# Performance work log

Measured on AMD Instinct MI355X. Metric: run time of the kernel, lower is better.

## Reference

```python
import jax, jax.numpy as jnp
import numpy as np

NH, DH, DM = 16, 128, 2048
ROPE_THETA = 10000.0


def setup_inputs() -> dict:
    key = jax.random.key(0)
    k1, k2, k3 = jax.random.split(key, 3)
    x = jax.random.normal(k1, (2, 2048, DM), dtype=jnp.float32)
    w_qkv = jax.random.normal(k2, (3 * DM, DM), dtype=jnp.float32) * (DM ** -0.5)
    w_op = jax.random.normal(k3, (DM, DM), dtype=jnp.float32) * (DM ** -0.5)
    return {"x": x, "w_qkv": w_qkv, "w_op": w_op}


def _rope_tables(T, dtype):
    inv_freq = 1.0 / (ROPE_THETA ** (jnp.arange(0, DH, 2, dtype=jnp.float32) / DH))
    t = jnp.arange(T, dtype=jnp.float32)
    freqs = jnp.outer(t, inv_freq)              # (T, DH/2)
    emb = jnp.concatenate([freqs, freqs], axis=-1)  # (T, DH)
    cos = jnp.cos(emb)[None, :, None, :].astype(dtype)  # (1,T,1,DH)
    sin = jnp.sin(emb)[None, :, None, :].astype(dtype)
    return cos, sin


def _rotate_half(a):
    a1, a2 = a[..., : DH // 2], a[..., DH // 2 :]
    return jnp.concatenate([-a2, a1], axis=-1)


def reference(x, w_qkv, w_op):
    B, T, D = x.shape
    qkv = jnp.einsum('btd,ed->bte', x, w_qkv).reshape(B, T, 3, NH, DH)
    q, k, v = qkv[:, :, 0], qkv[:, :, 1], qkv[:, :, 2]  # (B,T,NH,DH)

    cos, sin = _rope_tables(T, x.dtype)
    q = q * cos + _rotate_half(q) * sin
    k = k * cos + _rotate_half(k) * sin

    # causal scaled dot-product attention
    scale = 1.0 / jnp.sqrt(jnp.asarray(DH, dtype=x.dtype))
    scores = jnp.einsum('bqhd,bkhd->bhqk', q, k) * scale  # (B,NH,T,T)
    causal = jnp.tril(jnp.ones((T, T), dtype=bool))
    scores = jnp.where(causal[None, None], scores, jnp.asarray(-1e30, dtype=x.dtype))
    attn = jax.nn.softmax(scores, axis=-1)
    out = jnp.einsum('bhqk,bkhd->bqhd', attn, v).reshape(B, T, D)
    return jnp.einsum('btd,ed->bte', out, w_op)
```

## Files before the change

### kernel.cpp

```cpp
#include <hip/hip_runtime.h>
#include <hip/hip_bf16.h>
#include <cstdint>

#define NHEAD 16
#define DHEAD 128
#define DMODEL 2048
#define TSEQ 2048
#define BATCH 2

using bf16 = __hip_bfloat16;
typedef __attribute__((ext_vector_type(4))) float  f32x4;
typedef __attribute__((ext_vector_type(2))) float  f32x2;
typedef __attribute__((ext_vector_type(4))) float  float4_t;
typedef __attribute__((ext_vector_type(4))) short  s16x4;
typedef __bf16 bf16x8 __attribute__((ext_vector_type(8)));

#define GLOAD_LDS16(gptr, lptr)                                                        \
  __builtin_amdgcn_global_load_lds((const __attribute__((address_space(1))) void*)(gptr), \
                                   (__attribute__((address_space(3))) void*)(lptr), 16, 0, 0)

#if __has_builtin(__builtin_amdgcn_exp2f)
#define EXP2(x) __builtin_amdgcn_exp2f(x)
#else
#define EXP2(x) exp2f(x)
#endif

__device__ __forceinline__ float bf2f(bf16 v) { return __bfloat162float(v); }
__device__ __forceinline__ bf16  f2bf(float f) { return __float2bfloat16(f); }
__device__ __forceinline__ unsigned short bfbits(float f) {
  return __builtin_bit_cast(unsigned short, f2bf(f));
}
__device__ __forceinline__ unsigned int pack2(float a, float b) {
  return (unsigned int)bfbits(a) | ((unsigned int)bfbits(b) << 16);
}

__global__ void cast_f32_to_bf16(const float* __restrict__ in, unsigned short* __restrict__ out, int n4) {
  int stride = gridDim.x * blockDim.x;
  for (int i = blockIdx.x * blockDim.x + threadIdx.x; i < n4; i += stride) {
    float4_t v = reinterpret_cast<const float4_t*>(in)[i];
    s16x4 r;
    r.x = (short)bfbits(v.x);
    r.y = (short)bfbits(v.y);
    r.z = (short)bfbits(v.z);
    r.w = (short)bfbits(v.w);
    reinterpret_cast<s16x4*>(out)[i] = r;
  }
}

__global__ void rope_tables(f32x2* __restrict__ cstab) {
  int i = blockIdx.x * blockDim.x + threadIdx.x;
  if (i >= TSEQ * 64) return;
  int t = i >> 6, f = i & 63;
  float inv = __expf(-((2.0f * (float)f) / 128.0f) * logf(10000.0f));
  float ang = (float)t * inv;
  f32x2 cs;
  cs.x = cosf(ang);
  cs.y = sinf(ang);
  cstab[i] = cs;
}

__global__ void transpose_v(const unsigned short* __restrict__ qkv, unsigned short* __restrict__ vt) {
  __shared__ short tile[64][132];
  const int bh = blockIdx.y;
  const int b = bh >> 4, h = bh & 15;
  const int t0 = blockIdx.x * 64;
  const int tid = threadIdx.x;
#pragma unroll
  for (int p = 0; p < 8; ++p) {
    int row  = p * 8 + (tid >> 5);
    int col  = (tid & 31) * 4;
    const unsigned short* src = qkv + (size_t)(b * TSEQ + t0 + row) * (3 * DMODEL) + 2 * DMODEL + h * DHEAD + col;
    s16x4 v = *reinterpret_cast<const s16x4*>(src);
    *reinterpret_cast<s16x4*>(&tile[row][col]) = v;
  }
  __syncthreads();
#pragma unroll
  for (int q = 0; q < 8; ++q) {
    int idx = q * 256 + tid;
    int d = idx >> 4, tq = idx & 15;
    s16x4 r;
    r.x = tile[tq * 4 + 0][d];
    r.y = tile[tq * 4 + 1][d];
    r.z = tile[tq * 4 + 2][d];
    r.w = tile[tq * 4 + 3][d];
    *reinterpret_cast<s16x4*>(vt + (size_t)(bh * DHEAD + d) * TSEQ + t0 + tq * 4) = r;
  }
}

__device__ __forceinline__ void store_c(float* p, float v) { *p = v; }
__device__ __forceinline__ void store_c(unsigned short* p, float v) { *p = bfbits(v); }

template <typename CT, bool ROPE>
__global__ __launch_bounds__(512, 2) void gemm_8p(const unsigned short* __restrict__ A,
                                                  const unsigned short* __restrict__ B,
                                                  CT* __restrict__ C, int M, int N, int K,
                                                  const f32x2* __restrict__ cstab) {
  __shared__ __align__(16) unsigned short As[2][256 * 64];
  __shared__ __align__(16) unsigned short Bs[2][256 * 64];

  const int tid  = threadIdx.x;
  const int lane = tid & 63;
  const int wave = tid >> 6;
  const int lrow = lane >> 4, lcol = lane & 15;
  const int wm2 = wave >> 2, wn4 = wave & 3;

  const int cpx = gridDim.x >> 3;
  const int bid = (blockIdx.x & 7) * cpx + (blockIdx.x >> 3);
  const int nby = N >> 8;
  const int m0 = (bid / nby) * 256;
  const int n0 = (bid % nby) * 256;
  const int NT = K >> 6;

  f32x4 acc[8][4] = {};

#define STAGE_M(MAT, DST, slot, k0)                                          \
  {                                                                          \
    _Pragma("unroll")                                                        \
    for (int it_ = 0; it_ < 4; ++it_) {                                      \
      int CC_ = it_ * 512 + tid;                                             \
      int R_ = CC_ >> 3, c_ = CC_ & 7;                                       \
      GLOAD_LDS16(MAT + (size_t)((DST) + R_) * K + (k0) + ((c_ ^ (R_ & 7)) << 3), \
                  (char*)(&slot[0]) + CC_ * 16);                             \
    }                                                                        \
  }

#define RD_FRAG(BASE, R, ks)                                                 \
  (*reinterpret_cast<const bf16x8*>(                                         \
      (BASE) + (R) * 128 + (((((ks) << 2) + lrow) ^ (lcol & 7)) << 4)))

  STAGE_M(A, m0, As[0], 0);
  STAGE_M(B, n0, Bs[0], 0);
  __syncthreads();

  for (int t = 0; t < NT; ++t) {
    const char* Ab = (const char*)(&As[t & 1][0]);
    const char* Bb = (const char*)(&Bs[t & 1][0]);
    const bool pf = (t + 1 < NT);
    const int psl = (t + 1) & 1;
    const int pk0 = (t + 1) << 6;

    bf16x8 af[4][2], bfr[2][2];

#pragma unroll
    for (int mf = 0; mf < 4; ++mf)
#pragma unroll
      for (int ks = 0; ks < 2; ++ks)
        af[mf][ks] = RD_FRAG(Ab, wm2 * 128 + mf * 16 + lcol, ks);
#pragma unroll
    for (int si = 0; si < 2; ++si)
#pragma unroll
      for (int ks = 0; ks < 2; ++ks)
        bfr[si][ks] = RD_FRAG(Bb, (wn4 + 4 * si) * 16 + lcol, ks);
    if (pf) STAGE_M(A, m0, As[psl], pk0);
    __builtin_amdgcn_s_barrier();
    __builtin_amdgcn_sched_barrier(0);
    __builtin_amdgcn_s_setprio(1);
#pragma unroll
    for (int mf = 0; mf < 4; ++mf)
#pragma unroll
      for (int si = 0; si < 2; ++si)
#pragma unroll
        for (int ks = 0; ks < 2; ++ks)
          acc[mf][si] = __builtin_amdgcn_mfma_f32_16x16x32_bf16(af[mf][ks], bfr[si][ks], acc[mf][si], 0, 0, 0);
    __builtin_amdgcn_s_setprio(0);
    __builtin_amdgcn_s_barrier();
    __builtin_amdgcn_sched_barrier(0);

#pragma unroll
    for (int si = 0; si < 2; ++si)
#pragma unroll
      for (int ks = 0; ks < 2; ++ks)
        bfr[si][ks] = RD_FRAG(Bb, (wn4 + 4 * (2 + si)) * 16 + lcol, ks);
    if (pf) STAGE_M(B, n0, Bs[psl], pk0);
    __builtin_amdgcn_s_barrier();
    __builtin_amdgcn_sched_barrier(0);
    __builtin_amdgcn_s_setprio(1);
#pragma unroll
    for (int mf = 0; mf < 4; ++mf)
#pragma unroll
      for (int si = 0; si < 2; ++si)
#pragma unroll
        for (int ks = 0; ks < 2; ++ks)
          acc[mf][2 + si] = __builtin_amdgcn_mfma_f32_16x16x32_bf16(af[mf][ks], bfr[si][ks], acc[mf][2 + si], 0, 0, 0);
    __builtin_amdgcn_s_setprio(0);
    __builtin_amdgcn_s_barrier();
    __builtin_amdgcn_sched_barrier(0);

#pragma unroll
    for (int mf = 0; mf < 4; ++mf)
#pragma unroll
      for (int ks = 0; ks < 2; ++ks)
        af[mf][ks] = RD_FRAG(Ab, wm2 * 128 + (4 + mf) * 16 + lcol, ks);
    __builtin_amdgcn_s_barrier();
    __builtin_amdgcn_sched_barrier(0);
    __builtin_amdgcn_s_setprio(1);
#pragma unroll
    for (int mf = 0; mf < 4; ++mf)
#pragma unroll
      for (int si = 0; si < 2; ++si)
#pragma unroll
        for (int ks = 0; ks < 2; ++ks)
          acc[4 + mf][2 + si] = __builtin_amdgcn_mfma_f32_16x16x32_bf16(af[mf][ks], bfr[si][ks], acc[4 + mf][2 + si], 0, 0, 0);
    __builtin_amdgcn_s_setprio(0);
    __builtin_amdgcn_s_barrier();
    __builtin_amdgcn_sched_barrier(0);

#pragma unroll
    for (int si = 0; si < 2; ++si)
#pragma unroll
      for (int ks = 0; ks < 2; ++ks)
        bfr[si][ks] = RD_FRAG(Bb, (wn4 + 4 * si) * 16 + lcol, ks);
    __builtin_amdgcn_s_barrier();
    __builtin_amdgcn_sched_barrier(0);
    __builtin_amdgcn_s_setprio(1);
#pragma unroll
    for (int mf = 0; mf < 4; ++mf)
#pragma unroll
      for (int si = 0; si < 2; ++si)
#pragma unroll
        for (int ks = 0; ks < 2; ++ks)
          acc[4 + mf][si] = __builtin_amdgcn_mfma_f32_16x16x32_bf16(af[mf][ks], bfr[si][ks], acc[4 + mf][si], 0, 0, 0);
    __builtin_amdgcn_s_setprio(0);

    __syncthreads();
  }
#undef STAGE_M
#undef RD_FRAG

  if (ROPE && n0 < 2 * DMODEL) {
    const float qsc = (n0 < DMODEL) ? 0.12751743f : 1.0f;
    const int f = wn4 * 16 + lcol;
#pragma unroll
    for (int mi = 0; mi < 8; ++mi)
#pragma unroll
      for (int j = 0; j < 4; ++j) {
        const int r = m0 + wm2 * 128 + mi * 16 + lrow * 4 + j;
        const int t = r & (TSEQ - 1);
        const f32x2 cs = cstab[t * 64 + f];
        const float a1 = acc[mi][0][j], a2 = acc[mi][1][j];
        store_c(C + (size_t)r * N + n0 + f,       (a1 * cs.x - a2 * cs.y) * qsc);
        store_c(C + (size_t)r * N + n0 + f + 64,  (a2 * cs.x + a1 * cs.y) * qsc);
        const float b1 = acc[mi][2][j], b2 = acc[mi][3][j];
        store_c(C + (size_t)r * N + n0 + f + 128, (b1 * cs.x - b2 * cs.y) * qsc);
        store_c(C + (size_t)r * N + n0 + f + 192, (b2 * cs.x + b1 * cs.y) * qsc);
      }
  } else {
#pragma unroll
    for (int mi = 0; mi < 8; ++mi)
#pragma unroll
      for (int si = 0; si < 4; ++si)
#pragma unroll
        for (int j = 0; j < 4; ++j) {
          const int r = m0 + wm2 * 128 + mi * 16 + lrow * 4 + j;
          const int c = n0 + (wn4 + 4 * si) * 16 + lcol;
          store_c(C + (size_t)r * N + c, acc[mi][si][j]);
        }
  }
}

template <typename CT>
__global__ __launch_bounds__(256, 2) void gemm_bt(const unsigned short* __restrict__ A,
                                                  const unsigned short* __restrict__ B,
                                                  CT* __restrict__ C, int M, int N, int K) {
  __shared__ unsigned short As[128 * 32];
  __shared__ unsigned short Bs[128 * 32];
  const int tid  = threadIdx.x;
  const int wave = tid >> 6, lane = tid & 63;
  const int m0 = blockIdx.x * 128, n0 = blockIdx.y * 128;
  const int wm = wave * 32;
  const int lrow = lane >> 4, lcol = lane & 15;
  f32x4 acc[2][8] = {};

  for (int k0 = 0; k0 < K; k0 += 32) {
#pragma unroll
    for (int it = 0; it < 2; ++it) {
      int chunk = wave * 2 + it;
      int eoff  = chunk * 512 + lane * 8;
      int row   = eoff >> 5, col = eoff & 31;
      GLOAD_LDS16(A + (size_t)(m0 + row) * K + k0 + col, As + chunk * 512);
      GLOAD_LDS16(B + (size_t)(n0 + row) * K + k0 + col, Bs + chunk * 512);
    }
    __syncthreads();
    bf16x8 af[2], bfr[8];
#pragma unroll
    for (int mi = 0; mi < 2; ++mi)
      af[mi] = *reinterpret_cast<const bf16x8*>(&As[(wm + mi * 16 + lcol) * 32 + lrow * 8]);
#pragma unroll
    for (int ni = 0; ni < 8; ++ni)
      bfr[ni] = *reinterpret_cast<const bf16x8*>(&Bs[(ni * 16 + lcol) * 32 + lrow * 8]);
#pragma unroll
    for (int mi = 0; mi < 2; ++mi)
#pragma unroll
      for (int ni = 0; ni < 8; ++ni)
        acc[mi][ni] = __builtin_amdgcn_mfma_f32_16x16x32_bf16(af[mi], bfr[ni], acc[mi][ni], 0, 0, 0);
    __syncthreads();
  }
#pragma unroll
  for (int mi = 0; mi < 2; ++mi)
#pragma unroll
    for (int ni = 0; ni < 8; ++ni)
#pragma unroll
      for (int j = 0; j < 4; ++j) {
        int r = m0 + wm + mi * 16 + lrow * 4 + j;
        int c = n0 + ni * 16 + lcol;
        store_c(C + (size_t)r * N + c, acc[mi][ni][j]);
      }
}

__global__ __launch_bounds__(512, 4) void flash_attn(const unsigned short* __restrict__ qkv,
                                                     const unsigned short* __restrict__ vt,
                                                     unsigned short* __restrict__ out) {
  __shared__ unsigned short kb[2][64 * 128];
  __shared__ unsigned short vb[2][128 * 64];
  __shared__ unsigned short plds[8][16 * 64];

  const int tid  = threadIdx.x;
  const int wave = tid >> 6, lane = tid & 63;
  const int lrow = lane >> 4, lcol = lane & 15;
  const int h = blockIdx.y, b = blockIdx.z;
  const int q0b = blockIdx.x * 128;
  const int q0w = q0b + wave * 16;
  const size_t qkbase = (size_t)b * TSEQ * (3 * DMODEL);
  const unsigned short* kptr = qkv + qkbase + DMODEL + h * DHEAD;
  const unsigned short* vptr = vt + (size_t)((b * NHEAD + h) * DHEAD) * TSEQ;

  bf16x8 qf[4];
#pragma unroll
  for (int kk = 0; kk < 4; ++kk)
    qf[kk] = *reinterpret_cast<const bf16x8*>(
        qkv + qkbase + (size_t)(q0w + lcol) * (3 * DMODEL) + h * DHEAD + kk * 32 + lrow * 8);

  f32x4 o[8] = {};
  float m = -1.0e30f, l = 0.f;

  const int nsteps = 2 * blockIdx.x + 2;

#define STAGE_KV(bi, kv0s)                                                              \
  {                                                                                     \
    _Pragma("unroll")                                                                   \
    for (int c = 0; c < 2; ++c) {                                                       \
      int cc = c * 512 + tid;                                                           \
      int krow = cc >> 4, kchk = (cc & 15) ^ (krow & 7);                                \
      GLOAD_LDS16(kptr + (size_t)((kv0s) + krow) * (3 * DMODEL) + kchk * 8,             \
                  &kb[bi][cc * 8]);                                                     \
      int vrow = cc >> 3, vchk = (cc & 7) ^ (vrow & 7);                                 \
      GLOAD_LDS16(vptr + (size_t)vrow * TSEQ + (kv0s) + vchk * 8,                       \
                  &vb[bi][cc * 8]);                                                     \
    }                                                                                   \
  }

  STAGE_KV(0, 0);
  __syncthreads();

  int cur = 0;
  for (int s = 0; s < nsteps; ++s) {
    const int kv0 = s * 64;
    if (s + 1 < nsteps) STAGE_KV(cur ^ 1, kv0 + 64);

    if (kv0 <= q0w + 15) {
      const unsigned short* kbc = kb[cur];
      const unsigned short* vbc = vb[cur];

      f32x4 sc[4] = {};
      __builtin_amdgcn_s_setprio(1);
#pragma unroll
      for (int n = 0; n < 4; ++n) {
        const int r = n * 16 + lcol;
#pragma unroll
        for (int kk = 0; kk < 4; ++kk) {
          bf16x8 kf = *reinterpret_cast<const bf16x8*>(
              &kbc[r * 128 + (((kk * 4 + lrow) ^ (lcol & 7)) << 3)]);
          sc[n] = __builtin_amdgcn_mfma_f32_16x16x32_bf16(kf, qf[kk], sc[n], 0, 0, 0);
        }
      }
      __builtin_amdgcn_s_setprio(0);

      const bool diag = (kv0 + 63 > q0w);
      const int qi = q0w + lcol;
      float sv[16];
#pragma unroll
      for (int n = 0; n < 4; ++n)
#pragma unroll
        for (int j = 0; j < 4; ++j) {
          float v = sc[n][j];
          if (diag && (kv0 + n * 16 + lrow * 4 + j) > qi) v = -1.0e30f;
          sv[n * 4 + j] = v;
        }
      float t8[8];
#pragma unroll
      for (int j = 0; j < 8; ++j) t8[j] = fmaxf(sv[j], sv[j + 8]);
#pragma unroll
      for (int j = 0; j < 4; ++j) t8[j] = fmaxf(t8[j], t8[j + 4]);
      float pm = fmaxf(fmaxf(t8[0], t8[1]), fmaxf(t8[2], t8[3]));
      pm = fmaxf(pm, __shfl_xor(pm, 16));
      pm = fmaxf(pm, __shfl_xor(pm, 32));

      if (__any(pm > m + 11.5f)) {
        const float mn  = fmaxf(m, pm);
        const float fsc = EXP2(m - mn);
        m = mn;
        l *= fsc;
#pragma unroll
        for (int c = 0; c < 8; ++c) o[c] *= fsc;
      }

#pragma unroll
      for (int i = 0; i < 16; ++i) sv[i] = EXP2(sv[i] - m);
      float a8[8];
#pragma unroll
      for (int j = 0; j < 8; ++j) a8[j] = sv[j] + sv[j + 8];
#pragma unroll
      for (int j = 0; j < 4; ++j) a8[j] += a8[j + 4];
      float rs = (a8[0] + a8[1]) + (a8[2] + a8[3]);
      rs += __shfl_xor(rs, 16);
      rs += __shfl_xor(rs, 32);
      l += rs;

      char* pw = reinterpret_cast<char*>(&plds[wave][0]);
#pragma unroll
      for (int n = 0; n < 4; ++n)
#pragma unroll
        for (int j = 0; j < 4; j += 2) {
          int boff = (lcol << 7) + ((((n << 1) + (lrow >> 1)) ^ (lcol & 7)) << 4) +
                     ((lrow & 1) << 3) + (j << 1);
          *reinterpret_cast<unsigned int*>(pw + boff) = pack2(sv[n * 4 + j], sv[n * 4 + j + 1]);
        }
      asm volatile("s_waitcnt lgkmcnt(0)" ::: "memory");

      bf16x8 pf0 = *reinterpret_cast<const bf16x8*>(
          pw + (lcol << 7) + ((lrow ^ (lcol & 7)) << 4));
      bf16x8 pf1 = *reinterpret_cast<const bf16x8*>(
          pw + (lcol << 7) + (((4 + lrow) ^ (lcol & 7)) << 4));

      __builtin_amdgcn_s_setprio(1);
#pragma unroll
      for (int c = 0; c < 8; ++c) {
        const int d = c * 16 + lcol;
        bf16x8 vf0 = *reinterpret_cast<const bf16x8*>(
            &vbc[d * 64 + ((lrow ^ (lcol & 7)) << 3)]);
        o[c] = __builtin_amdgcn_mfma_f32_16x16x32_bf16(vf0, pf0, o[c], 0, 0, 0);
        bf16x8 vf1 = *reinterpret_cast<const bf16x8*>(
            &vbc[d * 64 + (((4 + lrow) ^ (lcol & 7)) << 3)]);
        o[c] = __builtin_amdgcn_mfma_f32_16x16x32_bf16(vf1, pf1, o[c], 0, 0, 0);
      }
      __builtin_amdgcn_s_setprio(0);
    }

    __syncthreads();
    cur ^= 1;
  }

  const float rl = 1.0f / l;
  const int trow = q0w + lcol;
#pragma unroll
  for (int c = 0; c < 8; ++c) {
    s16x4 st;
#pragma unroll
    for (int j = 0; j < 4; ++j) st[j] = (short)bfbits(o[c][j] * rl);
    *reinterpret_cast<s16x4*>(
        out + (size_t)(b * TSEQ + trow) * DMODEL + h * DHEAD + c * 16 + lrow * 4) = st;
  }
#undef STAGE_KV
}

extern "C" void kernel_launch(void* const* d_in, const int* in_sizes, int n_in,
                              void* d_out, int out_size, void* d_ws, size_t ws_size,
                              hipStream_t stream) {
  const float* x     = (const float*)d_in[0];
  const float* w_qkv = (const float*)d_in[1];
  const float* w_op  = (const float*)d_in[2];
  float* out = (float*)d_out;

  const size_t SZ_XB  = (size_t)4096 * 2048 * 2;
  const size_t SZ_WQ  = (size_t)6144 * 2048 * 2;
  const size_t SZ_WO  = (size_t)2048 * 2048 * 2;
  const size_t SZ_QKV = (size_t)4096 * 6144 * 2;
  const size_t SZ_VT  = (size_t)32 * 128 * 2048 * 2;
  const size_t SZ_AO  = (size_t)4096 * 2048 * 2;
  const size_t SZ_TAB = (size_t)2048 * 64 * 8;
  const size_t NEEDED = SZ_XB + SZ_WQ + SZ_WO + SZ_QKV + SZ_VT + SZ_AO + SZ_TAB;
  if (ws_size < NEEDED) return;

  char* p = (char*)d_ws;
  unsigned short* xb   = (unsigned short*)p; p += SZ_XB;
  unsigned short* wqb  = (unsigned short*)p; p += SZ_WQ;
  unsigned short* wob  = (unsigned short*)p; p += SZ_WO;
  unsigned short* qkv  = (unsigned short*)p; p += SZ_QKV;
  unsigned short* vt   = (unsigned short*)p; p += SZ_VT;
  unsigned short* ao   = (unsigned short*)p; p += SZ_AO;
  f32x2* cstab = (f32x2*)p; p += SZ_TAB;

  cast_f32_to_bf16<<<dim3(2048), dim3(256), 0, stream>>>(x, xb, 4096 * 2048 / 4);
  cast_f32_to_bf16<<<dim3(2048), dim3(256), 0, stream>>>(w_qkv, wqb, 6144 * 2048 / 4);
  cast_f32_to_bf16<<<dim3(2048), dim3(256), 0, stream>>>(w_op, wob, 2048 * 2048 / 4);
  rope_tables<<<dim3(512), dim3(256), 0, stream>>>(cstab);

  gemm_8p<unsigned short, true><<<dim3(384), dim3(512), 0, stream>>>(
      xb, wqb, qkv, 4096, 6144, 2048, cstab);
  transpose_v<<<dim3(32, 32), dim3(256), 0, stream>>>(qkv, vt);
  flash_attn<<<dim3(16, 16, 2), dim3(512), 0, stream>>>(qkv, vt, ao);
  gemm_bt<float><<<dim3(32, 16), dim3(256), 0, stream>>>(ao, wob, out, 4096, 2048, 2048);
}
```

Before: 300.8 us.

## Split GEMM tile prefetch into half-tiles with fine-grained vmcnt waits

Replaces the two whole-tile global-to-LDS prefetches per K step with four half-tile loads spread across the four MFMA phases. Explicit s_waitcnt vmcnt(2) waits replace the full __syncthreads at the end of each iteration, so only the oldest outstanding loads must finish before the next stage. The aim is to overlap global loads with MFMA work more evenly and cut barrier stalls. The correctness of the vmcnt accounting (two loads per thread per half-tile) is subtle and could cause LDS races if the ordering assumptions are off.

```diff
diff --git a/kernel.cpp b/kernel.cpp
--- a/kernel.cpp
+++ b/kernel.cpp
@@ -113,24 +113,31 @@
 
   f32x4 acc[8][4] = {};
 
-#define STAGE_M(MAT, DST, slot, k0)                                          \
-  {                                                                          \
-    _Pragma("unroll")                                                        \
-    for (int it_ = 0; it_ < 4; ++it_) {                                      \
-      int CC_ = it_ * 512 + tid;                                             \
-      int R_ = CC_ >> 3, c_ = CC_ & 7;                                       \
-      GLOAD_LDS16(MAT + (size_t)((DST) + R_) * K + (k0) + ((c_ ^ (R_ & 7)) << 3), \
-                  (char*)(&slot[0]) + CC_ * 16);                             \
-    }                                                                        \
+#define STAGE_H(MAT, BASE, slot, h, k0)                                           \
+  {                                                                               \
+    _Pragma("unroll")                                                             \
+    for (int it_ = 0; it_ < 2; ++it_) {                                           \
+      int CC_ = it_ * 512 + tid;                                                  \
+      int R_ = (h) * 128 + (CC_ >> 3), c_ = CC_ & 7;                              \
+      GLOAD_LDS16(MAT + (size_t)((BASE) + R_) * K + (k0) + ((c_ ^ (R_ & 7)) << 3),\
+                  (char*)(&slot[0]) + (h) * 16384 + CC_ * 16);                    \
+    }                                                                             \
   }
 
 #define RD_FRAG(BASE, R, ks)                                                 \
   (*reinterpret_cast<const bf16x8*>(                                         \
       (BASE) + (R) * 128 + (((((ks) << 2) + lrow) ^ (lcol & 7)) << 4)))
 
-  STAGE_M(A, m0, As[0], 0);
-  STAGE_M(B, n0, Bs[0], 0);
-  __syncthreads();
+#define WAITV2 asm volatile("s_waitcnt vmcnt(2)" ::: "memory")
+#define WAITV0 asm volatile("s_waitcnt vmcnt(0)" ::: "memory")
+#define BAR    { __builtin_amdgcn_s_barrier(); __builtin_amdgcn_sched_barrier(0); }
+
+  STAGE_H(A, m0, As[0], 0, 0);
+  STAGE_H(A, m0, As[0], 1, 0);
+  STAGE_H(B, n0, Bs[0], 0, 0);
+  STAGE_H(B, n0, Bs[0], 1, 0);
+  WAITV2;
+  BAR;
 
   for (int t = 0; t < NT; ++t) {
     const char* Ab = (const char*)(&As[t & 1][0]);
@@ -151,9 +158,8 @@
 #pragma unroll
       for (int ks = 0; ks < 2; ++ks)
         bfr[si][ks] = RD_FRAG(Bb, (wn4 + 4 * si) * 16 + lcol, ks);
-    if (pf) STAGE_M(A, m0, As[psl], pk0);
-    __builtin_amdgcn_s_barrier();
-    __builtin_amdgcn_sched_barrier(0);
+    if (pf) { STAGE_H(A, m0, As[psl], 0, pk0); WAITV2; } else { WAITV0; }
+    BAR;
     __builtin_amdgcn_s_setprio(1);
 #pragma unroll
     for (int mf = 0; mf < 4; ++mf)
@@ -163,17 +169,15 @@
         for (int ks = 0; ks < 2; ++ks)
           acc[mf][si] = __builtin_amdgcn_mfma_f32_16x16x32_bf16(af[mf][ks], bfr[si][ks], acc[mf][si], 0, 0, 0);
     __builtin_amdgcn_s_setprio(0);
-    __builtin_amdgcn_s_barrier();
-    __builtin_amdgcn_sched_barrier(0);
+    BAR;
 
 #pragma unroll
     for (int si = 0; si < 2; ++si)
 #pragma unroll
       for (int ks = 0; ks < 2; ++ks)
         bfr[si][ks] = RD_FRAG(Bb, (wn4 + 4 * (2 + si)) * 16 + lcol, ks);
-    if (pf) STAGE_M(B, n0, Bs[psl], pk0);
-    __builtin_amdgcn_s_barrier();
-    __builtin_amdgcn_sched_barrier(0);
+    if (pf) STAGE_H(A, m0, As[psl], 1, pk0);
+    BAR;
     __builtin_amdgcn_s_setprio(1);
 #pragma unroll
     for (int mf = 0; mf < 4; ++mf)
@@ -183,16 +187,15 @@
         for (int ks = 0; ks < 2; ++ks)
           acc[mf][2 + si] = __builtin_amdgcn_mfma_f32_16x16x32_bf16(af[mf][ks], bfr[si][ks], acc[mf][2 + si], 0, 0, 0);
     __builtin_amdgcn_s_setprio(0);
-    __builtin_amdgcn_s_barrier();
-    __builtin_amdgcn_sched_barrier(0);
+    BAR;
 
 #pragma unroll
     for (int mf = 0; mf < 4; ++mf)
 #pragma unroll
       for (int ks = 0; ks < 2; ++ks)
         af[mf][ks] = RD_FRAG(Ab, wm2 * 128 + (4 + mf) * 16 + lcol, ks);
-    __builtin_amdgcn_s_barrier();
-    __builtin_amdgcn_sched_barrier(0);
+    if (pf) STAGE_H(B, n0, Bs[psl], 0, pk0);
+    BAR;
     __builtin_amdgcn_s_setprio(1);
 #pragma unroll
     for (int mf = 0; mf < 4; ++mf)
@@ -202,16 +205,15 @@
         for (int ks = 0; ks < 2; ++ks)
           acc[4 + mf][2 + si] = __builtin_amdgcn_mfma_f32_16x16x32_bf16(af[mf][ks], bfr[si][ks], acc[4 + mf][2 + si], 0, 0, 0);
     __builtin_amdgcn_s_setprio(0);
-    __builtin_amdgcn_s_barrier();
-    __builtin_amdgcn_sched_barrier(0);
+    BAR;
 
 #pragma unroll
     for (int si = 0; si < 2; ++si)
 #pragma unroll
       for (int ks = 0; ks < 2; ++ks)
         bfr[si][ks] = RD_FRAG(Bb, (wn4 + 4 * si) * 16 + lcol, ks);
-    __builtin_amdgcn_s_barrier();
-    __builtin_amdgcn_sched_barrier(0);
+    if (pf) STAGE_H(B, n0, Bs[psl], 1, pk0);
+    BAR;
     __builtin_amdgcn_s_setprio(1);
 #pragma unroll
     for (int mf = 0; mf < 4; ++mf)
@@ -222,10 +224,14 @@
           acc[4 + mf][si] = __builtin_amdgcn_mfma_f32_16x16x32_bf16(af[mf][ks], bfr[si][ks], acc[4 + mf][si], 0, 0, 0);
     __builtin_amdgcn_s_setprio(0);
 
-    __syncthreads();
-  }
-#undef STAGE_M
+    if (pf) { WAITV2; } 
+    BAR;
+  }
+#undef STAGE_H
 #undef RD_FRAG
+#undef WAITV2
+#undef WAITV0
+#undef BAR
 
   if (ROPE && n0 < 2 * DMODEL) {
     const float qsc = (n0 < DMODEL) ? 0.12751743f : 1.0f;
```

New measurement: 306.1 us. Within noise of the previous version (+1.8%).
